# Kernel tuning notes

Measured on AMD Instinct MI355X. Metric: run time of the kernel, lower is better.

The kernel has to match this reference:

```python
import jax, jax.numpy as jnp
import numpy as np

D_MODEL = 2048
NUM_HEADS = 16
HEAD_DIM = D_MODEL // NUM_HEADS
B, T = 2, 2048


def setup_inputs() -> dict:
    key = jax.random.key(0)
    ks = jax.random.split(key, 6)
    x = jax.random.normal(ks[0], (B, T, D_MODEL), dtype=jnp.float32)
    # RoPE tables: angles theta_i = 10000^(-2i/d), half-dim tables [T, HEAD_DIM//2]
    pos = jnp.arange(T, dtype=jnp.float32)[:, None]
    inv_freq = 1.0 / (10000.0 ** (jnp.arange(0, HEAD_DIM, 2, dtype=jnp.float32) / HEAD_DIM))
    ang = pos * inv_freq[None, :]
    sin = jnp.sin(ang)
    cos = jnp.cos(ang)
    doc_ids = jnp.sort(jax.random.randint(ks[1], (B, T), 0, 4), axis=-1).astype(jnp.int32)
    W_qkv = jax.random.normal(ks[2], (D_MODEL, D_MODEL + 2 * HEAD_DIM), dtype=jnp.float32) * 0.02
    W_out = jax.random.normal(ks[3], (D_MODEL, D_MODEL), dtype=jnp.float32) * 0.02
    return {"x": x, "sin": sin, "cos": cos, "doc_ids": doc_ids, "W_qkv": W_qkv, "W_out": W_out}


def _apply_rope(x, sin, cos):
    # x: [..., T, ..., HEAD_DIM]; sin/cos: [T, HEAD_DIM//2], broadcast to x's rank
    if x.ndim == 4:  # [B, T, H, D]
        s, c = sin[None, :, None, :], cos[None, :, None, :]
    else:  # [B, T, D]
        s, c = sin[None, :, :], cos[None, :, :]
    x1, x2 = jnp.split(x, 2, axis=-1)
    return jnp.concatenate([x1 * c - x2 * s, x2 * c + x1 * s], axis=-1)


def reference(x, sin, cos, doc_ids, W_qkv, W_out):
    b, t, _ = x.shape
    qkv = x @ W_qkv  # [B, T, D_MODEL + 2*HEAD_DIM]
    q = qkv[..., :D_MODEL].reshape(b, t, NUM_HEADS, HEAD_DIM)
    k = qkv[..., D_MODEL:D_MODEL + HEAD_DIM]  # [B, T, HEAD_DIM] single KV head
    v = qkv[..., D_MODEL + HEAD_DIM:]         # [B, T, HEAD_DIM]
    q = _apply_rope(q, sin, cos)
    k = _apply_rope(k, sin, cos)
    # doc-packed causal mask -> additive bias [B, 1, T, T]
    neg_inf = jnp.finfo(q.dtype).min / 2
    causal = jnp.tril(jnp.ones((t, t), dtype=jnp.bool_))
    same_doc = doc_ids[:, :, None] == doc_ids[:, None, :]
    mask = (causal[None, :, :] & same_doc)[:, None, :, :]
    bias = jnp.where(mask, jnp.array(0.0, q.dtype), neg_inf)
    scale = 1.0 / jnp.sqrt(jnp.array(HEAD_DIM, q.dtype))
    scores = jnp.einsum("bthd,bsd->bhts", q, k) * scale + bias  # [B, H, T, T]
    attn = jax.nn.softmax(scores, axis=-1)
    out = jnp.einsum("bhts,bsd->bthd", attn, v).reshape(b, t, D_MODEL)
    return out @ W_out
```

## Files before the change

### kernel.cpp

```cpp
#include <hip/hip_runtime.h>
#include <math.h>

#define D_MODEL 2048
#define NUM_HEADS 16
#define HEAD_DIM 128
#define BB 2
#define TT 2048
#define QKV_N 2304
#define KOFF 2048
#define VOFF 2176

typedef __attribute__((ext_vector_type(8))) short short8;
typedef __attribute__((ext_vector_type(4))) float f32x4;

static __device__ __forceinline__ short f2bf(float f) {
  union { float f; unsigned u; } x; x.f = f;
  unsigned r = (x.u + 0x7FFFu + ((x.u >> 16) & 1u)) >> 16;
  return (short)r;
}
static __device__ __forceinline__ float bf2f(unsigned short u) {
  return __uint_as_float(((unsigned)u) << 16);
}

#define GLD16(gp, lp)                                              \
  __builtin_amdgcn_global_load_lds(                                \
      (const __attribute__((address_space(1))) void*)(gp),         \
      (__attribute__((address_space(3))) void*)(lp), 16, 0, 0)

template <bool OUT_BF16>
__global__ __launch_bounds__(256) void gemm_mfma_bt(
    const short* __restrict__ A, const short* __restrict__ Bt,
    void* __restrict__ Cv, int M, int N, int K)
{
  __shared__ short As[128 * 32];
  __shared__ short Bs[128 * 32];

  const int tid = threadIdx.x;
  const int w = tid >> 6, l = tid & 63;
  const int quad = l >> 4, l16 = l & 15;
  const int wm = w >> 1, wn = w & 1;
  const int m0 = blockIdx.y * 128, n0 = blockIdx.x * 128;

  f32x4 acc[4][4];
#pragma unroll
  for (int i = 0; i < 4; i++)
#pragma unroll
    for (int j = 0; j < 4; j++) acc[i][j] = (f32x4){0.f, 0.f, 0.f, 0.f};

  const short* aA = A + (size_t)(m0 + w * 32 + (l >> 2)) * K + (l & 3) * 8;
  const short* aB = Bt + (size_t)(n0 + w * 32 + (l >> 2)) * K + (l & 3) * 8;
  short* lA0 = As + (w * 2) * 512;
  short* lA1 = As + (w * 2 + 1) * 512;
  short* lB0 = Bs + (w * 2) * 512;
  short* lB1 = Bs + (w * 2 + 1) * 512;

  const short* Ard = As + (size_t)(wm * 64 + l16) * 32 + quad * 8;
  const short* Brd = Bs + (size_t)(wn * 64 + l16) * 32 + quad * 8;

  for (int k0 = 0; k0 < K; k0 += 32) {
    __syncthreads();
    GLD16(aA + k0, lA0);
    GLD16(aA + k0 + (size_t)16 * K, lA1);
    GLD16(aB + k0, lB0);
    GLD16(aB + k0 + (size_t)16 * K, lB1);
    __syncthreads();

    short8 af[4], bf[4];
#pragma unroll
    for (int mi = 0; mi < 4; mi++) af[mi] = *(const short8*)(Ard + mi * 16 * 32);
#pragma unroll
    for (int ni = 0; ni < 4; ni++) bf[ni] = *(const short8*)(Brd + ni * 16 * 32);
#pragma unroll
    for (int mi = 0; mi < 4; mi++)
#pragma unroll
      for (int ni = 0; ni < 4; ni++)
        acc[mi][ni] =
            __builtin_amdgcn_mfma_f32_16x16x32_bf16(af[mi], bf[ni], acc[mi][ni], 0, 0, 0);
  }

#pragma unroll
  for (int mi = 0; mi < 4; mi++) {
#pragma unroll
    for (int ni = 0; ni < 4; ni++) {
#pragma unroll
      for (int r = 0; r < 4; r++) {
        const int row = m0 + wm * 64 + mi * 16 + quad * 4 + r;
        const int col = n0 + wn * 64 + ni * 16 + l16;
        if constexpr (OUT_BF16)
          ((short*)Cv)[(size_t)row * N + col] = f2bf(acc[mi][ni][r]);
        else
          ((float*)Cv)[(size_t)row * N + col] = acc[mi][ni][r];
      }
    }
  }
}

__global__ __launch_bounds__(256) void convert_x(
    const float* __restrict__ x, short* __restrict__ xb)
{
  const size_t i4 = (size_t)blockIdx.x * 256 + threadIdx.x;
  float4 v = *(const float4*)(x + i4 * 4);
  short4 o;
  o.x = f2bf(v.x); o.y = f2bf(v.y); o.z = f2bf(v.z); o.w = f2bf(v.w);
  *(short4*)(xb + i4 * 4) = o;
}

__global__ __launch_bounds__(256) void transpose_w_bf(
    const float* __restrict__ W, short* __restrict__ Wt, int K, int N)
{
  __shared__ float t[32][33];
  const int tx = threadIdx.x, ty = threadIdx.y;
  const int n0 = blockIdx.x * 32, k0 = blockIdx.y * 32;
#pragma unroll
  for (int j = 0; j < 4; j++)
    t[ty + j * 8][tx] = W[(size_t)(k0 + ty + j * 8) * N + n0 + tx];
  __syncthreads();
#pragma unroll
  for (int j = 0; j < 4; j++)
    Wt[(size_t)(n0 + ty + j * 8) * K + k0 + tx] = f2bf(t[tx][ty + j * 8]);
}

__global__ __launch_bounds__(256) void rope_bf(
    short* __restrict__ qkv, const float* __restrict__ sin_t,
    const float* __restrict__ cos_t)
{
  const int idx = blockIdx.x * 256 + threadIdx.x;
  const int pairs_per_row = (NUM_HEADS + 1) * 64;
  const int total = BB * TT * pairs_per_row;
  if (idx >= total) return;
  const int p  = idx % pairs_per_row;
  const int bt = idx / pairs_per_row;
  const int t  = bt % TT;
  const int h  = p >> 6;
  const int i  = p & 63;
  const float s = sin_t[t * 64 + i];
  const float c = cos_t[t * 64 + i];
  short* base = qkv + (size_t)bt * QKV_N + h * HEAD_DIM;
  const float x1 = bf2f((unsigned short)base[i]);
  const float x2 = bf2f((unsigned short)base[64 + i]);
  base[i]      = f2bf(x1 * c - x2 * s);
  base[64 + i] = f2bf(x2 * c + x1 * s);
}

__global__ __launch_bounds__(256) void transpose_v(
    const short* __restrict__ qkv, short* __restrict__ Vtb)
{
  const int s = blockIdx.x * 256 + threadIdx.x;
  const int n = blockIdx.y;
  const int b = blockIdx.z;
  Vtb[((size_t)(b * 128 + n) << 11) + s] =
      qkv[(size_t)(b * TT + s) * QKV_N + VOFF + n];
}

#define KSTR 136
#define VSTR 72
#define PSTR 72

__global__ __launch_bounds__(256) void attn_mfma(
    const short* __restrict__ qkv, const short* __restrict__ Vtb,
    const int* __restrict__ doc_ids, short* __restrict__ attn_out)
{
  __shared__ short Ks[64 * KSTR];
  __shared__ short Vt[128 * VSTR];
  __shared__ short Pbuf[4 * 16 * PSTR];
  __shared__ int doc_s[64];

  const int qt = blockIdx.x, h = blockIdx.y, b = blockIdx.z;
  const int q0 = qt * 64;
  const int tid = threadIdx.x;
  const int w = tid >> 6;
  const int lane = tid & 63;
  const int quad = lane >> 4, l16 = lane & 15;

  const short* qp = qkv + (size_t)(b * TT + q0 + w * 16 + l16) * QKV_N
                    + h * HEAD_DIM + quad * 8;
  short8 Qf[4];
#pragma unroll
  for (int kc = 0; kc < 4; kc++) Qf[kc] = *(const short8*)(qp + kc * 32);

  const int docmin_q = doc_ids[b * TT + q0];
  const int docmax_q = doc_ids[b * TT + q0 + 63];

  int qg[4], mydoc[4];
  float l_i[4];
#pragma unroll
  for (int r = 0; r < 4; r++) {
    qg[r] = q0 + w * 16 + quad * 4 + r;
    mydoc[r] = doc_ids[b * TT + qg[r]];
    l_i[r] = 0.f;
  }
  f32x4 O[8];
#pragma unroll
  for (int v8 = 0; v8 < 8; v8++) O[v8] = (f32x4){0.f, 0.f, 0.f, 0.f};

  short* Pw = Pbuf + w * 16 * PSTR;
  const float scale = 0.08838834764831844f;

  for (int st = 0; st <= qt; st++) {
    const int s0 = st * 64;
    const int dmin_s = doc_ids[b * TT + s0];
    const int dmax_s = doc_ids[b * TT + s0 + 63];
    if (dmax_s < docmin_q) continue;
    const bool full = (st < qt) && (dmin_s == docmax_q);

    __syncthreads();
#pragma unroll
    for (int i = 0; i < 4; i++) {
      int f = i * 256 + tid;
      int row = f >> 4, seg = f & 15;
      int4 v = *(const int4*)(qkv + (size_t)(b * TT + s0 + row) * QKV_N + KOFF + seg * 8);
      *(int4*)(Ks + row * KSTR + seg * 8) = v;
    }
#pragma unroll
    for (int i = 0; i < 4; i++) {
      int f = i * 256 + tid;
      int n = f >> 3, seg = f & 7;
      int4 v = *(const int4*)(Vtb + ((size_t)(b * 128 + n) << 11) + s0 + seg * 8);
      *(int4*)(Vt + n * VSTR + seg * 8) = v;
    }
    if (!full && tid < 64) doc_s[tid] = doc_ids[b * TT + s0 + tid];
    __syncthreads();

    f32x4 S[4];
#pragma unroll
    for (int ns = 0; ns < 4; ns++) {
      f32x4 acc = (f32x4){0.f, 0.f, 0.f, 0.f};
      const short* kr = Ks + (ns * 16 + l16) * KSTR + quad * 8;
#pragma unroll
      for (int kc = 0; kc < 4; kc++) {
        short8 kf = *(const short8*)(kr + kc * 32);
        acc = __builtin_amdgcn_mfma_f32_16x16x32_bf16(Qf[kc], kf, acc, 0, 0, 0);
      }
      S[ns] = acc;
    }

    if (full) {
#pragma unroll
      for (int ns = 0; ns < 4; ns++)
#pragma unroll
        for (int r = 0; r < 4; r++) {
          const float p = __expf(S[ns][r] * scale);
          l_i[r] += p;
          Pw[(quad * 4 + r) * PSTR + ns * 16 + l16] = f2bf(p);
        }
    } else {
#pragma unroll
      for (int ns = 0; ns < 4; ns++) {
        const int s_loc = ns * 16 + l16;
        const int sg = s0 + s_loc;
        const int sdoc = doc_s[s_loc];
#pragma unroll
        for (int r = 0; r < 4; r++) {
          const bool ok = (sg <= qg[r]) && (sdoc == mydoc[r]);
          const float p = ok ? __expf(S[ns][r] * scale) : 0.f;
          l_i[r] += p;
          Pw[(quad * 4 + r) * PSTR + ns * 16 + l16] = f2bf(p);
        }
      }
    }

#pragma unroll
    for (int ks = 0; ks < 2; ks++) {
      short8 pf = *(const short8*)(Pw + l16 * PSTR + ks * 32 + quad * 8);
#pragma unroll
      for (int v8 = 0; v8 < 8; v8++) {
        short8 vf = *(const short8*)(Vt + (v8 * 16 + l16) * VSTR + ks * 32 + quad * 8);
        O[v8] = __builtin_amdgcn_mfma_f32_16x16x32_bf16(pf, vf, O[v8], 0, 0, 0);
      }
    }
  }

#pragma unroll
  for (int off = 8; off >= 1; off >>= 1)
#pragma unroll
    for (int r = 0; r < 4; r++) l_i[r] += __shfl_xor(l_i[r], off);

#pragma unroll
  for (int r = 0; r < 4; r++) {
    const float inv = 1.f / l_i[r];
    short* op = attn_out + (size_t)(b * TT + qg[r]) * D_MODEL + h * HEAD_DIM + l16;
#pragma unroll
    for (int v8 = 0; v8 < 8; v8++)
      op[v8 * 16] = f2bf(O[v8][r] * inv);
  }
}

extern "C" void kernel_launch(void* const* d_in, const int* in_sizes, int n_in,
                              void* d_out, int out_size, void* d_ws, size_t ws_size,
                              hipStream_t stream)
{
  const float* x     = (const float*)d_in[0];
  const float* sin_t = (const float*)d_in[1];
  const float* cos_t = (const float*)d_in[2];
  const int*   doc   = (const int*)  d_in[3];
  const float* W_qkv = (const float*)d_in[4];
  const float* W_out = (const float*)d_in[5];
  float* out = (float*)d_out;

  const int M = BB * TT;

  char* p = (char*)d_ws;
  short* qkv_bf = (short*)p; p += (size_t)M * QKV_N * 2;
  short* xb     = (short*)p; p += (size_t)M * D_MODEL * 2;
  short* attn_bf = xb;
  short* Vtb    = (short*)p; p += (size_t)BB * 128 * TT * 2;
  short* Wqkv_t = (short*)p; p += (size_t)QKV_N * D_MODEL * 2;
  short* Wout_t = (short*)p;

  convert_x<<<(M * D_MODEL / 4) / 256, 256, 0, stream>>>(x, xb);
  {
    dim3 grid(QKV_N / 32, D_MODEL / 32), blk(32, 8);
    transpose_w_bf<<<grid, blk, 0, stream>>>(W_qkv, Wqkv_t, D_MODEL, QKV_N);
  }
  {
    dim3 grid(D_MODEL / 32, D_MODEL / 32), blk(32, 8);
    transpose_w_bf<<<grid, blk, 0, stream>>>(W_out, Wout_t, D_MODEL, D_MODEL);
  }
  {
    dim3 grid(QKV_N / 128, M / 128);
    gemm_mfma_bt<true><<<grid, 256, 0, stream>>>(xb, Wqkv_t, qkv_bf, M, QKV_N, D_MODEL);
  }
  {
    const int total = BB * TT * (NUM_HEADS + 1) * 64;
    rope_bf<<<(total + 255) / 256, 256, 0, stream>>>(qkv_bf, sin_t, cos_t);
  }
  {
    dim3 grid(TT / 256, HEAD_DIM, BB);
    transpose_v<<<grid, 256, 0, stream>>>(qkv_bf, Vtb);
  }
  {
    dim3 grid(TT / 64, NUM_HEADS, BB);
    attn_mfma<<<grid, 256, 0, stream>>>(qkv_bf, Vtb, doc, attn_bf);
  }
  {
    dim3 grid(D_MODEL / 128, M / 128);
    gemm_mfma_bt<false><<<grid, 256, 0, stream>>>(attn_bf, Wout_t, out, M, D_MODEL, D_MODEL);
  }
}
```

Measured before the change: 302.5 us.

## Fuse RoPE and V transpose into QKV GEMM epilogue, swizzle block order

```diff
diff --git a/kernel.cpp b/kernel.cpp
--- a/kernel.cpp
+++ b/kernel.cpp
@@ -27,19 +27,32 @@
       (const __attribute__((address_space(1))) void*)(gp),         \
       (__attribute__((address_space(3))) void*)(lp), 16, 0, 0)
 
-template <bool OUT_BF16>
-__global__ __launch_bounds__(256) void gemm_mfma_bt(
+static __device__ __forceinline__ void swizzle_xy(int& bx, int& by) {
+  const int gx = gridDim.x;
+  const int lin = blockIdx.y * gx + blockIdx.x;
+  const int band = lin / (gx * 8);
+  const int rem = lin - band * gx * 8;
+  by = band * 8 + (rem & 7);
+  bx = rem >> 3;
+}
+
+__global__ __launch_bounds__(256) void gemm_qkv_rope(
     const short* __restrict__ A, const short* __restrict__ Bt,
-    void* __restrict__ Cv, int M, int N, int K)
+    short* __restrict__ qkv, short* __restrict__ Vtb,
+    const float* __restrict__ sin_t, const float* __restrict__ cos_t)
 {
   __shared__ short As[128 * 32];
   __shared__ short Bs[128 * 32];
+  const int K = D_MODEL;
+
+  int bx, by;
+  swizzle_xy(bx, by);
 
   const int tid = threadIdx.x;
   const int w = tid >> 6, l = tid & 63;
   const int quad = l >> 4, l16 = l & 15;
   const int wm = w >> 1, wn = w & 1;
-  const int m0 = blockIdx.y * 128, n0 = blockIdx.x * 128;
+  const int m0 = by * 128, n0 = bx * 128;
 
   f32x4 acc[4][4];
 #pragma unroll
@@ -55,7 +68,7 @@
   short* lB1 = Bs + (w * 2 + 1) * 512;
 
   const short* Ard = As + (size_t)(wm * 64 + l16) * 32 + quad * 8;
-  const short* Brd = Bs + (size_t)(wn * 64 + l16) * 32 + quad * 8;
+  const short* Brd = Bs + (size_t)(wn * 16 + l16) * 32 + quad * 8;
 
   for (int k0 = 0; k0 < K; k0 += 32) {
     __syncthreads();
@@ -69,7 +82,7 @@
 #pragma unroll
     for (int mi = 0; mi < 4; mi++) af[mi] = *(const short8*)(Ard + mi * 16 * 32);
 #pragma unroll
-    for (int ni = 0; ni < 4; ni++) bf[ni] = *(const short8*)(Brd + ni * 16 * 32);
+    for (int ni = 0; ni < 4; ni++) bf[ni] = *(const short8*)(Brd + ni * 32 * 32);
 #pragma unroll
     for (int mi = 0; mi < 4; mi++)
 #pragma unroll
@@ -78,6 +91,88 @@
             __builtin_amdgcn_mfma_f32_16x16x32_bf16(af[mi], bf[ni], acc[mi][ni], 0, 0, 0);
   }
 
+  const int colbase = wn * 16 + l16;
+  const bool is_v = (n0 == VOFF);
+
+#pragma unroll
+  for (int mi = 0; mi < 4; mi++) {
+#pragma unroll
+    for (int r = 0; r < 4; r++) {
+      const int row = m0 + wm * 64 + mi * 16 + quad * 4 + r;
+      const int b = row >> 11, t = row & (TT - 1);
+#pragma unroll
+      for (int ni = 0; ni < 2; ni++) {
+        const int cloc = ni * 32 + colbase;
+        const float c1 = acc[mi][ni][r];
+        const float c2 = acc[mi][ni + 2][r];
+        if (!is_v) {
+          const float sn = sin_t[t * 64 + cloc];
+          const float cs = cos_t[t * 64 + cloc];
+          short* op = qkv + (size_t)row * QKV_N + n0 + cloc;
+          op[0]  = f2bf(c1 * cs - c2 * sn);
+          op[64] = f2bf(c2 * cs + c1 * sn);
+        } else {
+          Vtb[((size_t)(b * 128 + cloc) << 11) + t]      = f2bf(c1);
+          Vtb[((size_t)(b * 128 + cloc + 64) << 11) + t] = f2bf(c2);
+        }
+      }
+    }
+  }
+}
+
+__global__ __launch_bounds__(256) void gemm_mfma_bt(
+    const short* __restrict__ A, const short* __restrict__ Bt,
+    float* __restrict__ C, int M, int N, int K)
+{
+  __shared__ short As[128 * 32];
+  __shared__ short Bs[128 * 32];
+
+  int bx, by;
+  swizzle_xy(bx, by);
+
+  const int tid = threadIdx.x;
+  const int w = tid >> 6, l = tid & 63;
+  const int quad = l >> 4, l16 = l & 15;
+  const int wm = w >> 1, wn = w & 1;
+  const int m0 = by * 128, n0 = bx * 128;
+
+  f32x4 acc[4][4];
+#pragma unroll
+  for (int i = 0; i < 4; i++)
+#pragma unroll
+    for (int j = 0; j < 4; j++) acc[i][j] = (f32x4){0.f, 0.f, 0.f, 0.f};
+
+  const short* aA = A + (size_t)(m0 + w * 32 + (l >> 2)) * K + (l & 3) * 8;
+  const short* aB = Bt + (size_t)(n0 + w * 32 + (l >> 2)) * K + (l & 3) * 8;
+  short* lA0 = As + (w * 2) * 512;
+  short* lA1 = As + (w * 2 + 1) * 512;
+  short* lB0 = Bs + (w * 2) * 512;
+  short* lB1 = Bs + (w * 2 + 1) * 512;
+
+  const short* Ard = As + (size_t)(wm * 64 + l16) * 32 + quad * 8;
+  const short* Brd = Bs + (size_t)(wn * 64 + l16) * 32 + quad * 8;
+
+  for (int k0 = 0; k0 < K; k0 += 32) {
+    __syncthreads();
+    GLD16(aA + k0, lA0);
+    GLD16(aA + k0 + (size_t)16 * K, lA1);
+    GLD16(aB + k0, lB0);
+    GLD16(aB + k0 + (size_t)16 * K, lB1);
+    __syncthreads();
+
+    short8 af[4], bf[4];
+#pragma unroll
+    for (int mi = 0; mi < 4; mi++) af[mi] = *(const short8*)(Ard + mi * 16 * 32);
+#pragma unroll
+    for (int ni = 0; ni < 4; ni++) bf[ni] = *(const short8*)(Brd + ni * 16 * 32);
+#pragma unroll
+    for (int mi = 0; mi < 4; mi++)
+#pragma unroll
+      for (int ni = 0; ni < 4; ni++)
+        acc[mi][ni] =
+            __builtin_amdgcn_mfma_f32_16x16x32_bf16(af[mi], bf[ni], acc[mi][ni], 0, 0, 0);
+  }
+
 #pragma unroll
   for (int mi = 0; mi < 4; mi++) {
 #pragma unroll
@@ -86,10 +181,7 @@
       for (int r = 0; r < 4; r++) {
         const int row = m0 + wm * 64 + mi * 16 + quad * 4 + r;
         const int col = n0 + wn * 64 + ni * 16 + l16;
-        if constexpr (OUT_BF16)
-          ((short*)Cv)[(size_t)row * N + col] = f2bf(acc[mi][ni][r]);
-        else
-          ((float*)Cv)[(size_t)row * N + col] = acc[mi][ni][r];
+        C[(size_t)row * N + col] = acc[mi][ni][r];
       }
     }
   }
@@ -118,38 +210,6 @@
 #pragma unroll
   for (int j = 0; j < 4; j++)
     Wt[(size_t)(n0 + ty + j * 8) * K + k0 + tx] = f2bf(t[tx][ty + j * 8]);
-}
-
-__global__ __launch_bounds__(256) void rope_bf(
-    short* __restrict__ qkv, const float* __restrict__ sin_t,
-    const float* __restrict__ cos_t)
-{
-  const int idx = blockIdx.x * 256 + threadIdx.x;
-  const int pairs_per_row = (NUM_HEADS + 1) * 64;
-  const int total = BB * TT * pairs_per_row;
-  if (idx >= total) return;
-  const int p  = idx % pairs_per_row;
-  const int bt = idx / pairs_per_row;
-  const int t  = bt % TT;
-  const int h  = p >> 6;
-  const int i  = p & 63;
-  const float s = sin_t[t * 64 + i];
-  const float c = cos_t[t * 64 + i];
-  short* base = qkv + (size_t)bt * QKV_N + h * HEAD_DIM;
-  const float x1 = bf2f((unsigned short)base[i]);
-  const float x2 = bf2f((unsigned short)base[64 + i]);
-  base[i]      = f2bf(x1 * c - x2 * s);
-  base[64 + i] = f2bf(x2 * c + x1 * s);
-}
-
-__global__ __launch_bounds__(256) void transpose_v(
-    const short* __restrict__ qkv, short* __restrict__ Vtb)
-{
-  const int s = blockIdx.x * 256 + threadIdx.x;
-  const int n = blockIdx.y;
-  const int b = blockIdx.z;
-  Vtb[((size_t)(b * 128 + n) << 11) + s] =
-      qkv[(size_t)(b * TT + s) * QKV_N + VOFF + n];
 }
 
 #define KSTR 136
@@ -318,15 +378,7 @@
   }
   {
     dim3 grid(QKV_N / 128, M / 128);
-    gemm_mfma_bt<true><<<grid, 256, 0, stream>>>(xb, Wqkv_t, qkv_bf, M, QKV_N, D_MODEL);
-  }
-  {
-    const int total = BB * TT * (NUM_HEADS + 1) * 64;
-    rope_bf<<<(total + 255) / 256, 256, 0, stream>>>(qkv_bf, sin_t, cos_t);
-  }
-  {
-    dim3 grid(TT / 256, HEAD_DIM, BB);
-    transpose_v<<<grid, 256, 0, stream>>>(qkv_bf, Vtb);
+    gemm_qkv_rope<<<grid, 256, 0, stream>>>(xb, Wqkv_t, qkv_bf, Vtb, sin_t, cos_t);
   }
   {
     dim3 grid(TT / 64, NUM_HEADS, BB);
@@ -334,6 +386,6 @@
   }
   {
     dim3 grid(D_MODEL / 128, M / 128);
-    gemm_mfma_bt<false><<<grid, 256, 0, stream>>>(attn_bf, Wout_t, out, M, D_MODEL, D_MODEL);
-  }
-}
+    gemm_mfma_bt<<<grid, 256, 0, stream>>>(attn_bf, Wout_t, out, M, D_MODEL, D_MODEL);
+  }
+}
```

Result: faster. 287.5 us (-5.0%).
